# Kernel tuning notes

Measured on AMD Instinct MI355X. Metric: run time of the kernel, lower is better.

## Reference

```python
import jax, jax.numpy as jnp
import numpy as np

# Model dims (match init_kwargs)
E = 2048   # embed_dim
H = 16     # num_heads
QR = 512   # q_low_rank
KVR = 512  # kv_low_rank
DR = 64    # rope_dim
DV = 128   # v_head_dim
S = 2048   # seq_len


def _make_rotary(seq_len, dim):
    inv_freq = 1.0 / jnp.power(10000.0, jnp.arange(0, dim, 2, dtype=jnp.float32) / dim)
    t = jnp.arange(seq_len, dtype=jnp.float32)
    freqs = jnp.outer(t, inv_freq)  # (S, dim//2)
    return jnp.sin(freqs), jnp.cos(freqs)


def _apply_rope(x, sin, cos):
    # x: (S, H_or_1, D); sin/cos: (S, D//2)
    d = x.shape[-1] // 2
    x1, x2 = x[..., :d], x[..., d:]
    s = jnp.concatenate([sin, sin], axis=-1)[:, None, :]
    c = jnp.concatenate([cos, cos], axis=-1)[:, None, :]
    return x * c + jnp.concatenate([-x2, x1], axis=-1) * s


def setup_inputs() -> dict:
    key = jax.random.key(0)
    ks = jax.random.split(key, 8)
    def lin(k, out_dim, in_dim):
        return jax.random.normal(k, (out_dim, in_dim), dtype=jnp.float32) * (1.0 / np.sqrt(in_dim))
    return {
        "x": jax.random.normal(ks[0], (S, E), dtype=jnp.float32),
        "wq_down": lin(ks[1], QR, E),
        "wq_up": lin(ks[2], H * DV, QR),
        "wq_rope": lin(ks[3], H * DR, QR),
        "wkv_down": lin(ks[4], KVR, E),
        "wkv_up": lin(ks[5], H * 2 * DV, KVR),
        "wk_rope": lin(ks[6], DR, E),
        "wo": lin(ks[7], E, H * DV),
    }


def reference(x, wq_down, wq_up, wq_rope, wkv_down, wkv_up, wk_rope, wo):
    seq = x.shape[0]
    # Query path: low-rank bottleneck -> content + rope streams
    c_q = x @ wq_down.T                                   # (S, QR)
    q_content = (c_q @ wq_up.T).reshape(seq, H, DV)       # (S, H, DV)
    q_rope = (c_q @ wq_rope.T).reshape(seq, H, DR)        # (S, H, DR)
    # KV path: shared low-rank bottleneck
    c_kv = x @ wkv_down.T                                 # (S, KVR)
    kv = c_kv @ wkv_up.T                                  # (S, 2*H*DV)
    k_content_flat, v_flat = jnp.split(kv, 2, axis=-1)
    k_content = k_content_flat.reshape(seq, H, DV)
    v = v_flat.reshape(seq, H, DV)
    # Shared key-RoPE projection (one per position, broadcast over heads)
    k_rope_shared = (x @ wk_rope.T)[:, None, :]           # (S, 1, DR)
    sin, cos = _make_rotary(seq, DR)
    q_rope_rot = _apply_rope(q_rope, sin, cos)            # (S, H, DR)
    k_rope_rot = _apply_rope(k_rope_shared, sin, cos)     # (S, 1, DR)
    # Concat content + rope streams; QK head dim = DV + DR
    dt = jnp.bfloat16
    q = jnp.concatenate([q_content, q_rope_rot], axis=-1).astype(dt)                            # (S, H, DV+DR)
    k = jnp.concatenate([k_content, jnp.broadcast_to(k_rope_rot, (seq, H, DR))], axis=-1).astype(dt)
    v_attn = v.astype(dt)
    scale = 1.0 / np.sqrt(DV + DR)
    # Attention. Note: original zero-pads V to DV+DR then slices output back to
    # DV -- mathematically identical to attending with unpadded V.
    logits = jnp.einsum('shd,thd->hst', q, k).astype(jnp.float32) * scale  # (H, S, S)
    probs = jax.nn.softmax(logits, axis=-1).astype(dt)
    attn = jnp.einsum('hst,thd->shd', probs, v_attn)      # (S, H, DV)
    attn_flat = attn.reshape(seq, H * DV)
    return (attn_flat @ wo.T).astype(jnp.float32)         # (S, E)
```

## Files before the change

### kernel.cpp

```cpp
#include <hip/hip_runtime.h>
#include <stdint.h>
#include <math.h>

#define S_LEN 2048
#define NH 16

typedef __attribute__((ext_vector_type(8))) short bf16x8;
typedef __attribute__((ext_vector_type(4))) float f32x4;
typedef __attribute__((ext_vector_type(16))) float f32x16;
typedef unsigned short ush;

__device__ __forceinline__ ush f2bf(float f) {
  union { float f; unsigned u; } v; v.f = f;
  unsigned x = v.u;
  return (ush)((x + 0x7fffu + ((x >> 16) & 1u)) >> 16);
}
__device__ __forceinline__ float bf2f(ush b) {
  union { unsigned u; float f; } v; v.u = ((unsigned)b) << 16;
  return v.f;
}
__device__ __forceinline__ ush f2h(float f) {
  _Float16 h = (_Float16)f;
  union { _Float16 h; ush u; } v; v.h = h;
  return v.u;
}
__device__ __forceinline__ float h2f(ush u) {
  union { ush u; _Float16 h; } v; v.u = u;
  return (float)v.h;
}

__device__ __forceinline__ void gload_lds16(const ush* g, ush* l) {
  __builtin_amdgcn_global_load_lds((const __attribute__((address_space(1))) void*)g,
                                   (__attribute__((address_space(3))) void*)l, 16, 0, 0);
}

__global__ void mega_pack(const float* __restrict__ wq_down, const float* __restrict__ wkv_down,
                          const float* __restrict__ wk_rope, const float* __restrict__ wq_up,
                          const float* __restrict__ wq_rope, const float* __restrict__ wkv_up,
                          const float* __restrict__ wo, const float* __restrict__ x,
                          ush* __restrict__ wdh, ush* __restrict__ wqh, ush* __restrict__ wkvuh,
                          ush* __restrict__ woh, ush* __restrict__ xh, float* __restrict__ tab) {
  int idx = blockIdx.x * 256 + threadIdx.x;
  if (idx < 2359296) {
    int r = idx >> 11, c = idx & 2047;
    float v = (r < 512) ? wq_down[(size_t)r * 2048 + c]
            : (r < 1024) ? wkv_down[(size_t)(r - 512) * 2048 + c]
            : (r < 1088) ? wk_rope[(size_t)(r - 1024) * 2048 + c] : 0.f;
    wdh[idx] = f2h(v);
    return;
  }
  idx -= 2359296;
  if (idx < 1572864) {
    int r = idx >> 9, c = idx & 511;
    float v = (r < 2048) ? wq_up[(size_t)r * 512 + c] : wq_rope[(size_t)(r - 2048) * 512 + c];
    wqh[idx] = f2h(v);
    return;
  }
  idx -= 1572864;
  if (idx < 2097152) { wkvuh[idx] = f2h(wkv_up[idx]); return; }
  idx -= 2097152;
  if (idx < 4194304) { woh[idx] = f2h(wo[idx]); return; }
  idx -= 4194304;
  if (idx < 4194304) { xh[idx] = f2h(x[idx]); return; }
  idx -= 4194304;
  if (idx < 65536) {
    int tt = idx >> 5, i = idx & 31;
    float inv_freq = 1.0f / powf(10000.0f, (float)i * (1.0f / 32.0f));
    float fr = (float)tt * inv_freq;
    tab[idx] = sinf(fr);
    tab[65536 + idx] = cosf(fr);
  }
}

__global__ __launch_bounds__(256) void gemm_down(
    const ush* __restrict__ A, const ush* __restrict__ B,
    ush* __restrict__ cqh, ush* __restrict__ ckvh, float* __restrict__ krl) {
  constexpr int K = 2048;
  __shared__ __align__(16) ush As[2 * 64 * 32];
  __shared__ __align__(16) ush Bs[2 * 64 * 32];
  const int t = threadIdx.x, l = t & 63, w = t >> 6;
  const int wm = w & 1, wn = w >> 1;
  const int m0 = blockIdx.y * 64, n0 = blockIdx.x * 64;
  const int lm = l & 15, lq = l >> 4;
  const int lr = l >> 2, lc = (l & 3) * 8;

  f32x4 acc[2][2];
  const f32x4 zero = {0.f, 0.f, 0.f, 0.f};
#pragma unroll
  for (int i = 0; i < 2; i++)
#pragma unroll
    for (int j = 0; j < 2; j++) acc[i][j] = zero;

  const ush* Ag = A + (size_t)(m0 + w * 16 + lr) * K + lc;
  const ush* Bg = B + (size_t)(n0 + w * 16 + lr) * K + lc;

  gload_lds16(Ag, As + w * 512);
  gload_lds16(Bg, Bs + w * 512);

  int cur = 0;
  for (int k0 = 0; k0 < K; k0 += 32) {
    asm volatile("s_waitcnt vmcnt(0)" ::: "memory");
    __builtin_amdgcn_s_barrier();
    __builtin_amdgcn_sched_barrier(0);
    if (k0 + 32 < K) {
      int nb = cur ^ 1;
      gload_lds16(Ag + k0 + 32, As + nb * 2048 + w * 512);
      gload_lds16(Bg + k0 + 32, Bs + nb * 2048 + w * 512);
    }
    __builtin_amdgcn_sched_barrier(0);
    const ush* Asc = As + cur * 2048;
    const ush* Bsc = Bs + cur * 2048;
    bf16x8 af[2], bfr[2];
#pragma unroll
    for (int i = 0; i < 2; i++)
      af[i] = *(const bf16x8*)(Asc + (wm * 32 + i * 16 + lm) * 32 + lq * 8);
#pragma unroll
    for (int j = 0; j < 2; j++)
      bfr[j] = *(const bf16x8*)(Bsc + (wn * 32 + j * 16 + lm) * 32 + lq * 8);
#pragma unroll
    for (int i = 0; i < 2; i++)
#pragma unroll
      for (int j = 0; j < 2; j++)
        acc[i][j] = __builtin_amdgcn_mfma_f32_16x16x32_f16(af[i], bfr[j], acc[i][j], 0, 0, 0);
    cur ^= 1;
  }

#pragma unroll
  for (int i = 0; i < 2; i++)
#pragma unroll
    for (int j = 0; j < 2; j++)
#pragma unroll
      for (int r = 0; r < 4; r++) {
        int mm = m0 + wm * 32 + i * 16 + lq * 4 + r;
        int nn = n0 + wn * 32 + j * 16 + lm;
        float v = acc[i][j][r];
        if (nn < 512)       cqh[(size_t)mm * 512 + nn] = f2h(v);
        else if (nn < 1024) ckvh[(size_t)mm * 512 + nn - 512] = f2h(v);
        else if (nn < 1088) krl[(size_t)mm * 64 + nn - 1024] = v;
      }
}

__global__ __launch_bounds__(256) void gemm_up(
    const ush* __restrict__ cqh, const ush* __restrict__ wqh,
    const ush* __restrict__ ckvh, const ush* __restrict__ wkvuh,
    ush* __restrict__ qupf, ush* __restrict__ kvf) {
  constexpr int BM = 128, BN = 64, K = 512, FI = 4, FJ = 2;
  __shared__ __align__(16) ush As[2 * BM * 32];
  __shared__ __align__(16) ush Bs[2 * BN * 32];
  int bx = blockIdx.x;
  const ush* A; const ush* B; ush* C; int ldc;
  if (bx < 48) { A = cqh; B = wqh; C = qupf; ldc = 3072; }
  else { bx -= 48; A = ckvh; B = wkvuh; C = kvf; ldc = 4096; }
  const int t = threadIdx.x, l = t & 63, w = t >> 6;
  const int wm = w & 1, wn = w >> 1;
  const int m0 = blockIdx.y * BM, n0 = bx * BN;
  const int lm = l & 15, lq = l >> 4;
  const int lr = l >> 2, lc = (l & 3) * 8;

  f32x4 acc[FI][FJ];
  const f32x4 zero = {0.f, 0.f, 0.f, 0.f};
#pragma unroll
  for (int i = 0; i < FI; i++)
#pragma unroll
    for (int j = 0; j < FJ; j++) acc[i][j] = zero;

  const ush* Ag[2];
#pragma unroll
  for (int i = 0; i < 2; i++) Ag[i] = A + (size_t)(m0 + w * 32 + i * 16 + lr) * K + lc;
  const ush* Bg = B + (size_t)(n0 + w * 16 + lr) * K + lc;

#pragma unroll
  for (int i = 0; i < 2; i++) gload_lds16(Ag[i], As + w * 1024 + i * 512);
  gload_lds16(Bg, Bs + w * 512);

  int cur = 0;
  for (int k0 = 0; k0 < K; k0 += 32) {
    asm volatile("s_waitcnt vmcnt(0)" ::: "memory");
    __builtin_amdgcn_s_barrier();
    __builtin_amdgcn_sched_barrier(0);
    if (k0 + 32 < K) {
      int nb = cur ^ 1;
#pragma unroll
      for (int i = 0; i < 2; i++)
        gload_lds16(Ag[i] + k0 + 32, As + nb * 4096 + w * 1024 + i * 512);
      gload_lds16(Bg + k0 + 32, Bs + nb * 2048 + w * 512);
    }
    __builtin_amdgcn_sched_barrier(0);
    const ush* Asc = As + cur * 4096;
    const ush* Bsc = Bs + cur * 2048;
    bf16x8 af[FI], bfr[FJ];
#pragma unroll
    for (int i = 0; i < FI; i++)
      af[i] = *(const bf16x8*)(Asc + (wm * 64 + i * 16 + lm) * 32 + lq * 8);
#pragma unroll
    for (int j = 0; j < FJ; j++)
      bfr[j] = *(const bf16x8*)(Bsc + (wn * 32 + j * 16 + lm) * 32 + lq * 8);
#pragma unroll
    for (int i = 0; i < FI; i++)
#pragma unroll
      for (int j = 0; j < FJ; j++)
        acc[i][j] = __builtin_amdgcn_mfma_f32_16x16x32_f16(af[i], bfr[j], acc[i][j], 0, 0, 0);
    cur ^= 1;
  }

#pragma unroll
  for (int i = 0; i < FI; i++)
#pragma unroll
    for (int j = 0; j < FJ; j++)
#pragma unroll
      for (int r = 0; r < 4; r++) {
        int mm = m0 + wm * 64 + i * 16 + lq * 4 + r;
        int nn = n0 + wn * 32 + j * 16 + lm;
        C[(size_t)mm * ldc + nn] = f2h(acc[i][j][r]);
      }
}

__global__ __launch_bounds__(256) void gemm_out(
    const ush* __restrict__ A, const ush* __restrict__ B, float* __restrict__ C,
    int K, int ldc) {
  constexpr int BM = 128, BN = 64, FI = 4, FJ = 2;
  __shared__ __align__(16) ush As[2 * BM * 32];
  __shared__ __align__(16) ush Bs[2 * BN * 32];
  const int t = threadIdx.x, l = t & 63, w = t >> 6;
  const int wm = w & 1, wn = w >> 1;
  const int m0 = blockIdx.y * BM, n0 = blockIdx.x * BN;
  const int lm = l & 15, lq = l >> 4;
  const int lr = l >> 2, lc = (l & 3) * 8;

  f32x4 acc[FI][FJ];
  const f32x4 zero = {0.f, 0.f, 0.f, 0.f};
#pragma unroll
  for (int i = 0; i < FI; i++)
#pragma unroll
    for (int j = 0; j < FJ; j++) acc[i][j] = zero;

  const ush* Ag[2];
#pragma unroll
  for (int i = 0; i < 2; i++) Ag[i] = A + (size_t)(m0 + w * 32 + i * 16 + lr) * K + lc;
  const ush* Bg = B + (size_t)(n0 + w * 16 + lr) * K + lc;

#pragma unroll
  for (int i = 0; i < 2; i++) gload_lds16(Ag[i], As + w * 1024 + i * 512);
  gload_lds16(Bg, Bs + w * 512);

  int cur = 0;
  for (int k0 = 0; k0 < K; k0 += 32) {
    asm volatile("s_waitcnt vmcnt(0)" ::: "memory");
    __builtin_amdgcn_s_barrier();
    __builtin_amdgcn_sched_barrier(0);
    if (k0 + 32 < K) {
      int nb = cur ^ 1;
#pragma unroll
      for (int i = 0; i < 2; i++)
        gload_lds16(Ag[i] + k0 + 32, As + nb * 4096 + w * 1024 + i * 512);
      gload_lds16(Bg + k0 + 32, Bs + nb * 2048 + w * 512);
    }
    __builtin_amdgcn_sched_barrier(0);
    const ush* Asc = As + cur * 4096;
    const ush* Bsc = Bs + cur * 2048;
    bf16x8 af[FI], bfr[FJ];
#pragma unroll
    for (int i = 0; i < FI; i++)
      af[i] = *(const bf16x8*)(Asc + (wm * 64 + i * 16 + lm) * 32 + lq * 8);
#pragma unroll
    for (int j = 0; j < FJ; j++)
      bfr[j] = *(const bf16x8*)(Bsc + (wn * 32 + j * 16 + lm) * 32 + lq * 8);
#pragma unroll
    for (int i = 0; i < FI; i++)
#pragma unroll
      for (int j = 0; j < FJ; j++)
        acc[i][j] = __builtin_amdgcn_mfma_f32_16x16x32_f16(af[i], bfr[j], acc[i][j], 0, 0, 0);
    cur ^= 1;
  }

#pragma unroll
  for (int i = 0; i < FI; i++)
#pragma unroll
    for (int j = 0; j < FJ; j++)
#pragma unroll
      for (int r = 0; r < 4; r++) {
        int mm = m0 + wm * 64 + i * 16 + lq * 4 + r;
        int nn = n0 + wn * 32 + j * 16 + lm;
        C[(size_t)mm * ldc + nn] = acc[i][j][r];
      }
}

__global__ void build_all(const ush* __restrict__ qupf, const ush* __restrict__ kvf,
                          const float* __restrict__ krl, const float* __restrict__ tab,
                          ush* __restrict__ qb, ush* __restrict__ kbt, ush* __restrict__ vtt) {
  const float scale = 0.07216878364870323f;
  if (blockIdx.x >= 50176) {
    __shared__ ush Vt[128 * 72];
    int b = blockIdx.x - 50176;
    const int T = b & 31, h = b >> 5, t = threadIdx.x;
    const int key = t >> 5, d0 = (t & 31) * 4;
#pragma unroll
    for (int pass = 0; pass < 8; ++pass) {
      int k = key + pass * 8;
      int s = T * 64 + k;
      ushort4 v = *(const ushort4*)(kvf + (size_t)s * 4096 + 2048 + h * 128 + d0);
      Vt[(d0 + 0) * 72 + k] = f2bf(h2f(v.x));
      Vt[(d0 + 1) * 72 + k] = f2bf(h2f(v.y));
      Vt[(d0 + 2) * 72 + k] = f2bf(h2f(v.z));
      Vt[(d0 + 3) * 72 + k] = f2bf(h2f(v.w));
    }
    __syncthreads();
    ush* dst = vtt + (size_t)(h * 32 + T) * 9216;
    for (int off = t; off < 1152; off += 256) {
      int row = off / 9, c8 = (off % 9) * 8;
      *(bf16x8*)(dst + row * 72 + c8) = *(const bf16x8*)(Vt + row * 72 + c8);
    }
    return;
  }
  int idx = blockIdx.x * 256 + threadIdx.x;
  if (idx < 6291456) {
    int d = idx % 192; int sh = idx / 192; int h = sh & 15; int s = sh >> 4;
    ush v;
    if (d < 128) {
      v = f2bf(h2f(qupf[(size_t)s * 3072 + h * 128 + d]) * scale);
    } else {
      int r = d - 128, i = r & 31;
      float sn = tab[s * 32 + i], cs = tab[65536 + s * 32 + i];
      const ush* qr = qupf + (size_t)s * 3072 + 2048 + h * 64;
      float xv = h2f(qr[r]);
      float other = (r < 32) ? -h2f(qr[r + 32]) : h2f(qr[r - 32]);
      v = f2bf((xv * cs + other * sn) * scale);
    }
    qb[((size_t)h * S_LEN + s) * 192 + d] = v;
    return;
  }
  idx -= 6291456;
  if (idx < 6553600) {
    int c = idx % 200; int r2 = idx / 200;
    int key = r2 & 63; int r3 = r2 >> 6; int T = r3 & 31; int h = r3 >> 5;
    int s = T * 64 + key;
    ush v = 0;
    if (c < 128) {
      v = f2bf(h2f(kvf[(size_t)s * 4096 + h * 128 + c]));
    } else if (c < 192) {
      int r = c - 128, i = r & 31;
      float sn = tab[s * 32 + i], cs = tab[65536 + s * 32 + i];
      const float* kr = krl + (size_t)s * 64;
      float xv = kr[r];
      float other = (r < 32) ? -kr[r + 32] : kr[r - 32];
      v = f2bf(xv * cs + other * sn);
    }
    kbt[((size_t)(h * 32 + T) * 64 + key) * 200 + c] = v;
  }
}

__global__ __launch_bounds__(512, 2) void attn_fused(
    const ush* __restrict__ qb, const ush* __restrict__ kbt, const ush* __restrict__ vtt,
    ush* __restrict__ opart, float* __restrict__ ml) {
  __shared__ __align__(16) ush Ks[64 * 200];
  __shared__ __align__(16) ush Vs[2][128 * 72];
  const int t = threadIdx.x, l = t & 63, w = t >> 6;
  const int id = blockIdx.x + 8 * (blockIdx.y + 16 * blockIdx.z);
  const int wid = (id & 7) * 64 + (id >> 3);
  const int qx = wid & 7, h = (wid >> 3) & 15, z = wid >> 7;
  const int qrow0 = qx * 256 + w * 32;
  const int ln = l & 31, lh = l >> 5;

  bf16x8 qf[12];
#pragma unroll
  for (int st = 0; st < 12; st++)
    qf[st] = *(const bf16x8*)(qb + ((size_t)h * S_LEN + qrow0 + ln) * 192 + st * 16 + lh * 8);
#pragma unroll
  for (int st = 0; st < 12; st++) asm volatile("" : "+v"(qf[st]));

  f32x16 o[4];
#pragma unroll
  for (int i = 0; i < 4; i++)
#pragma unroll
    for (int r = 0; r < 16; r++) o[i][r] = 0.f;
  float ps = 0.f;

  const ush* kbase = kbt + (size_t)(h * 32 + z * 8) * 12800;
  const ush* vbase = vtt + (size_t)(h * 32 + z * 8) * 9216;

  auto smpack = [&ps](const f32x16& svv, bf16x8& f0, bf16x8& f1) {
    unsigned pk8[8];
#pragma unroll
    for (int g = 0; g < 4; g++) {
      float p0 = __expf(svv[4 * g + 0]);
      float p1 = __expf(svv[4 * g + 1]);
      float p2 = __expf(svv[4 * g + 2]);
      float p3 = __expf(svv[4 * g + 3]);
      ps += (p0 + p1) + (p2 + p3);
      unsigned lo, hi;
      asm("v_cvt_pk_bf16_f32 %0, %1, %2" : "=v"(lo) : "v"(p0), "v"(p1));
      asm("v_cvt_pk_bf16_f32 %0, %1, %2" : "=v"(hi) : "v"(p2), "v"(p3));
      pk8[2 * g] = lo; pk8[2 * g + 1] = hi;
    }
    asm("v_permlane32_swap_b32 %0, %1" : "+v"(pk8[0]), "+v"(pk8[2]));
    asm("v_permlane32_swap_b32 %0, %1" : "+v"(pk8[1]), "+v"(pk8[3]));
    asm("v_permlane32_swap_b32 %0, %1" : "+v"(pk8[4]), "+v"(pk8[6]));
    asm("v_permlane32_swap_b32 %0, %1" : "+v"(pk8[5]), "+v"(pk8[7]));
    union { unsigned d[4]; bf16x8 v; } u0, u1;
    u0.d[0] = pk8[0]; u0.d[1] = pk8[1]; u0.d[2] = pk8[2]; u0.d[3] = pk8[3];
    u1.d[0] = pk8[4]; u1.d[1] = pk8[5]; u1.d[2] = pk8[6]; u1.d[3] = pk8[7];
    f0 = u0.v; f1 = u1.v;
  };

  for (int c = w; c < 25; c += 8) gload_lds16(kbase + c * 512 + l * 8, &Ks[c * 512]);
  for (int c = w; c < 18; c += 8) gload_lds16(vbase + c * 512 + l * 8, &Vs[0][c * 512]);
  asm volatile("s_waitcnt vmcnt(0)" ::: "memory");
  __builtin_amdgcn_s_barrier();
  __builtin_amdgcn_sched_barrier(0);

  int cur = 0;
  for (int it = 0; it < 8; ++it) {
    const ush* Vb = &Vs[cur][0];

    f32x16 sv0, sv1;
#pragma unroll
    for (int r = 0; r < 16; r++) { sv0[r] = 0.f; sv1[r] = 0.f; }

    __builtin_amdgcn_s_setprio(1);
#pragma unroll
    for (int st = 0; st < 12; st++) {
      bf16x8 af = *(const bf16x8*)(Ks + ln * 200 + st * 16 + lh * 8);
      sv0 = __builtin_amdgcn_mfma_f32_32x32x16_bf16(af, qf[st], sv0, 0, 0, 0);
    }
    __builtin_amdgcn_s_setprio(0);

    bf16x8 pf00, pf01;
    smpack(sv0, pf00, pf01);

    __builtin_amdgcn_s_setprio(1);
#pragma unroll
    for (int st = 0; st < 12; st++) {
      bf16x8 af = *(const bf16x8*)(Ks + (32 + ln) * 200 + st * 16 + lh * 8);
      sv1 = __builtin_amdgcn_mfma_f32_32x32x16_bf16(af, qf[st], sv1, 0, 0, 0);
    }
    __builtin_amdgcn_s_setprio(0);

    __builtin_amdgcn_sched_barrier(0);
    __builtin_amdgcn_s_barrier();
    __builtin_amdgcn_sched_barrier(0);
    if (it < 7) {
      const ush* ksrc = kbase + (size_t)(it + 1) * 12800;
      const ush* vsrc = vbase + (size_t)(it + 1) * 9216;
      for (int c = w; c < 25; c += 8) gload_lds16(ksrc + c * 512 + l * 8, &Ks[c * 512]);
      ush* vd = &Vs[cur ^ 1][0];
      for (int c = w; c < 18; c += 8) gload_lds16(vsrc + c * 512 + l * 8, vd + c * 512);
    }
    __builtin_amdgcn_sched_barrier(0);

    __builtin_amdgcn_s_setprio(1);
#pragma unroll
    for (int db = 0; db < 4; db++) {
      bf16x8 vf0 = *(const bf16x8*)(Vb + (db * 32 + ln) * 72 + lh * 8);
      bf16x8 vf1 = *(const bf16x8*)(Vb + (db * 32 + ln) * 72 + 16 + lh * 8);
      o[db] = __builtin_amdgcn_mfma_f32_32x32x16_bf16(vf0, pf00, o[db], 0, 0, 0);
      o[db] = __builtin_amdgcn_mfma_f32_32x32x16_bf16(vf1, pf01, o[db], 0, 0, 0);
    }
    __builtin_amdgcn_s_setprio(0);

    bf16x8 pf10, pf11;
    smpack(sv1, pf10, pf11);

    __builtin_amdgcn_s_setprio(1);
#pragma unroll
    for (int db = 0; db < 4; db++) {
      bf16x8 vf0 = *(const bf16x8*)(Vb + (db * 32 + ln) * 72 + 32 + lh * 8);
      bf16x8 vf1 = *(const bf16x8*)(Vb + (db * 32 + ln) * 72 + 48 + lh * 8);
      o[db] = __builtin_amdgcn_mfma_f32_32x32x16_bf16(vf0, pf10, o[db], 0, 0, 0);
      o[db] = __builtin_amdgcn_mfma_f32_32x32x16_bf16(vf1, pf11, o[db], 0, 0, 0);
    }
    __builtin_amdgcn_s_setprio(0);

    __builtin_amdgcn_sched_barrier(0);
    asm volatile("s_waitcnt vmcnt(0)" ::: "memory");
    __builtin_amdgcn_s_barrier();
    __builtin_amdgcn_sched_barrier(0);
    cur ^= 1;
  }

  float lsum = ps + __shfl_xor(ps, 32, 64);
  const int s = qrow0 + ln;
  const size_t rbase = ((size_t)((z * 16 + h) * 2048) + s) * 128;
#pragma unroll
  for (int db = 0; db < 4; db++)
#pragma unroll
    for (int rq = 0; rq < 4; rq++) {
      ushort4 v4;
      v4.x = f2h(o[db][rq * 4 + 0] * 0.0625f);
      v4.y = f2h(o[db][rq * 4 + 1] * 0.0625f);
      v4.z = f2h(o[db][rq * 4 + 2] * 0.0625f);
      v4.w = f2h(o[db][rq * 4 + 3] * 0.0625f);
      *(ushort4*)(&opart[rbase + db * 32 + 8 * rq + 4 * lh]) = v4;
    }
  if (lh == 0) ml[(size_t)(z * 16 + h) * 2048 + s] = lsum;
}

__global__ __launch_bounds__(256) void attn_reduce(const ush* __restrict__ opart,
                                                   const float* __restrict__ ml,
                                                   ush* __restrict__ attnh) {
  int row = blockIdx.x * 4 + (threadIdx.x >> 6);
  int l = threadIdx.x & 63;
  int h = row >> 11, s = row & 2047;
  float lsum = 0.f;
#pragma unroll
  for (int z = 0; z < 4; z++) lsum += ml[(size_t)(z * 16 + h) * 2048 + s];
  float inv = 16.0f / lsum;
#pragma unroll
  for (int c0 = 0; c0 < 128; c0 += 64) {
    int c = c0 + l;
    float acc = 0.f;
#pragma unroll
    for (int z = 0; z < 4; z++)
      acc += h2f(opart[((size_t)(z * 16 + h) * 2048 + s) * 128 + c]);
    attnh[(size_t)s * 2048 + h * 128 + c] = f2h(bf2f(f2bf(acc * inv)));
  }
}

extern "C" void kernel_launch(void* const* d_in, const int* in_sizes, int n_in,
                              void* d_out, int out_size, void* d_ws, size_t ws_size,
                              hipStream_t stream) {
  const float* x        = (const float*)d_in[0];
  const float* wq_down  = (const float*)d_in[1];
  const float* wq_up    = (const float*)d_in[2];
  const float* wq_rope  = (const float*)d_in[3];
  const float* wkv_down = (const float*)d_in[4];
  const float* wkv_up   = (const float*)d_in[5];
  const float* wk_rope  = (const float*)d_in[6];
  const float* wo       = (const float*)d_in[7];
  char* ws = (char*)d_ws;

  size_t off = 0;
  auto alloc = [&](size_t b) { size_t c = off; off += (b + 255) & ~(size_t)255; return c; };
  const size_t XH    = alloc(2048UL * 2048 * 2);
  const size_t WDH   = alloc(1152UL * 2048 * 2);
  const size_t KRL   = alloc(2048UL * 64 * 4);
  const size_t CQH   = alloc(2048UL * 512 * 2);
  const size_t CKVH  = alloc(2048UL * 512 * 2);
  const size_t WQH   = alloc(3072UL * 512 * 2);
  const size_t QUPF  = alloc(2048UL * 3072 * 2);
  const size_t WKVUH = alloc(4096UL * 512 * 2);
  const size_t WOH   = alloc(2048UL * 2048 * 2);
  const size_t KVF   = alloc(2048UL * 4096 * 2);
  const size_t QB    = alloc(16UL * 2048 * 192 * 2);
  const size_t KBT   = alloc(16UL * 32 * 12800 * 2);
  const size_t VTT   = alloc(16UL * 32 * 9216 * 2);
  const size_t TAB   = alloc(2048UL * 32 * 4 * 2);
  const size_t OPART = alloc(4UL * 16 * 2048 * 128 * 2);
  const size_t ML    = alloc(4UL * 16 * 2048 * 4);
  const size_t ATTNH = XH;

  mega_pack<<<dim3(56576), 256, 0, stream>>>(
      wq_down, wkv_down, wk_rope, wq_up, wq_rope, wkv_up, wo, x,
      (ush*)(ws + WDH), (ush*)(ws + WQH), (ush*)(ws + WKVUH),
      (ush*)(ws + WOH), (ush*)(ws + XH), (float*)(ws + TAB));

  gemm_down<<<dim3(18, 32), 256, 0, stream>>>(
      (ush*)(ws + XH), (ush*)(ws + WDH),
      (ush*)(ws + CQH), (ush*)(ws + CKVH), (float*)(ws + KRL));

  gemm_up<<<dim3(112, 16), 256, 0, stream>>>(
      (ush*)(ws + CQH), (ush*)(ws + WQH),
      (ush*)(ws + CKVH), (ush*)(ws + WKVUH),
      (ush*)(ws + QUPF), (ush*)(ws + KVF));

  build_all<<<dim3(50688), 256, 0, stream>>>(
      (const ush*)(ws + QUPF), (const ush*)(ws + KVF), (const float*)(ws + KRL),
      (const float*)(ws + TAB), (ush*)(ws + QB), (ush*)(ws + KBT), (ush*)(ws + VTT));

  attn_fused<<<dim3(8, 16, 4), 512, 0, stream>>>(
      (ush*)(ws + QB), (ush*)(ws + KBT), (ush*)(ws + VTT),
      (ush*)(ws + OPART), (float*)(ws + ML));
  attn_reduce<<<dim3(8192), 256, 0, stream>>>((const ush*)(ws + OPART), (const float*)(ws + ML),
                                              (ush*)(ws + ATTNH));

  gemm_out<<<dim3(32, 16), 256, 0, stream>>>(
      (ush*)(ws + ATTNH), (ush*)(ws + WOH), (float*)d_out, 2048, 2048);
}
```

Measured before the change: 317.6 us.

## Double-buffer K in LDS and read V fragments directly from global memory

Removes the V tile staging in shared memory and loads V operand fragments for the PV matmul straight from global memory per wave. The freed LDS is used to double-buffer K, with the next K tile prefetched at the top of each iteration. The two barriers per iteration become one. This removes LDS write and barrier cost for V but adds redundant global/L2 reads of V across waves and exposes global latency on the PV MFMAs.

```diff
diff --git a/kernel.cpp b/kernel.cpp
--- a/kernel.cpp
+++ b/kernel.cpp
@@ -352,8 +352,7 @@
 __global__ __launch_bounds__(512, 2) void attn_fused(
     const ush* __restrict__ qb, const ush* __restrict__ kbt, const ush* __restrict__ vtt,
     ush* __restrict__ opart, float* __restrict__ ml) {
-  __shared__ __align__(16) ush Ks[64 * 200];
-  __shared__ __align__(16) ush Vs[2][128 * 72];
+  __shared__ __align__(16) ush Ks[2][64 * 200];
   const int t = threadIdx.x, l = t & 63, w = t >> 6;
   const int id = blockIdx.x + 8 * (blockIdx.y + 16 * blockIdx.z);
   const int wid = (id & 7) * 64 + (id >> 3);
@@ -377,6 +376,7 @@
 
   const ush* kbase = kbt + (size_t)(h * 32 + z * 8) * 12800;
   const ush* vbase = vtt + (size_t)(h * 32 + z * 8) * 9216;
+  const ush* vrow = vbase + ln * 72 + lh * 8;
 
   auto smpack = [&ps](const f32x16& svv, bf16x8& f0, bf16x8& f1) {
     unsigned pk8[8];
@@ -402,15 +402,22 @@
     f0 = u0.v; f1 = u1.v;
   };
 
-  for (int c = w; c < 25; c += 8) gload_lds16(kbase + c * 512 + l * 8, &Ks[c * 512]);
-  for (int c = w; c < 18; c += 8) gload_lds16(vbase + c * 512 + l * 8, &Vs[0][c * 512]);
-  asm volatile("s_waitcnt vmcnt(0)" ::: "memory");
-  __builtin_amdgcn_s_barrier();
-  __builtin_amdgcn_sched_barrier(0);
+  for (int c = w; c < 25; c += 8) gload_lds16(kbase + c * 512 + l * 8, &Ks[0][c * 512]);
 
   int cur = 0;
   for (int it = 0; it < 8; ++it) {
-    const ush* Vb = &Vs[cur][0];
+    asm volatile("s_waitcnt vmcnt(0)" ::: "memory");
+    __builtin_amdgcn_s_barrier();
+    __builtin_amdgcn_sched_barrier(0);
+    if (it < 7) {
+      const ush* ksrc = kbase + (size_t)(it + 1) * 12800;
+      ush* kd = &Ks[cur ^ 1][0];
+      for (int c = w; c < 25; c += 8) gload_lds16(ksrc + c * 512 + l * 8, kd + c * 512);
+    }
+    __builtin_amdgcn_sched_barrier(0);
+
+    const ush* Kb = &Ks[cur][0];
+    const ush* vt = vrow + (size_t)it * 9216;
 
     f32x16 sv0, sv1;
 #pragma unroll
@@ -419,7 +426,7 @@
     __builtin_amdgcn_s_setprio(1);
 #pragma unroll
     for (int st = 0; st < 12; st++) {
-      bf16x8 af = *(const bf16x8*)(Ks + ln * 200 + st * 16 + lh * 8);
+      bf16x8 af = *(const bf16x8*)(Kb + ln * 200 + st * 16 + lh * 8);
       sv0 = __builtin_amdgcn_mfma_f32_32x32x16_bf16(af, qf[st], sv0, 0, 0, 0);
     }
     __builtin_amdgcn_s_setprio(0);
@@ -430,28 +437,16 @@
     __builtin_amdgcn_s_setprio(1);
 #pragma unroll
     for (int st = 0; st < 12; st++) {
-      bf16x8 af = *(const bf16x8*)(Ks + (32 + ln) * 200 + st * 16 + lh * 8);
+      bf16x8 af = *(const bf16x8*)(Kb + (32 + ln) * 200 + st * 16 + lh * 8);
       sv1 = __builtin_amdgcn_mfma_f32_32x32x16_bf16(af, qf[st], sv1, 0, 0, 0);
     }
     __builtin_amdgcn_s_setprio(0);
 
-    __builtin_amdgcn_sched_barrier(0);
-    __builtin_amdgcn_s_barrier();
-    __builtin_amdgcn_sched_barrier(0);
-    if (it < 7) {
-      const ush* ksrc = kbase + (size_t)(it + 1) * 12800;
-      const ush* vsrc = vbase + (size_t)(it + 1) * 9216;
-      for (int c = w; c < 25; c += 8) gload_lds16(ksrc + c * 512 + l * 8, &Ks[c * 512]);
-      ush* vd = &Vs[cur ^ 1][0];
-      for (int c = w; c < 18; c += 8) gload_lds16(vsrc + c * 512 + l * 8, vd + c * 512);
-    }
-    __builtin_amdgcn_sched_barrier(0);
-
     __builtin_amdgcn_s_setprio(1);
 #pragma unroll
     for (int db = 0; db < 4; db++) {
-      bf16x8 vf0 = *(const bf16x8*)(Vb + (db * 32 + ln) * 72 + lh * 8);
-      bf16x8 vf1 = *(const bf16x8*)(Vb + (db * 32 + ln) * 72 + 16 + lh * 8);
+      bf16x8 vf0 = *(const bf16x8*)(vt + db * 2304);
+      bf16x8 vf1 = *(const bf16x8*)(vt + db * 2304 + 16);
       o[db] = __builtin_amdgcn_mfma_f32_32x32x16_bf16(vf0, pf00, o[db], 0, 0, 0);
       o[db] = __builtin_amdgcn_mfma_f32_32x32x16_bf16(vf1, pf01, o[db], 0, 0, 0);
     }
@@ -463,17 +458,13 @@
     __builtin_amdgcn_s_setprio(1);
 #pragma unroll
     for (int db = 0; db < 4; db++) {
-      bf16x8 vf0 = *(const bf16x8*)(Vb + (db * 32 + ln) * 72 + 32 + lh * 8);
-      bf16x8 vf1 = *(const bf16x8*)(Vb + (db * 32 + ln) * 72 + 48 + lh * 8);
+      bf16x8 vf0 = *(const bf16x8*)(vt + db * 2304 + 32);
+      bf16x8 vf1 = *(const bf16x8*)(vt + db * 2304 + 48);
       o[db] = __builtin_amdgcn_mfma_f32_32x32x16_bf16(vf0, pf10, o[db], 0, 0, 0);
       o[db] = __builtin_amdgcn_mfma_f32_32x32x16_bf16(vf1, pf11, o[db], 0, 0, 0);
     }
     __builtin_amdgcn_s_setprio(0);
 
-    __builtin_amdgcn_sched_barrier(0);
-    asm volatile("s_waitcnt vmcnt(0)" ::: "memory");
-    __builtin_amdgcn_s_barrier();
-    __builtin_amdgcn_sched_barrier(0);
     cur ^= 1;
   }
 
```

Measured after the change: 320.6 us. About the same (+0.9%).
